# Kernel optimization log

Hardware: AMD Instinct MI355X
Metric: run time of the kernel (lower is better)

The kernel has to match this reference:

```python
import jax, jax.numpy as jnp
import numpy as np

B, S, D = 2, 2048, 4096
H, KV = 32, 8
HD = D // H  # 128
REP = H // KV  # 4
THETA = 10000.0


def _rope(x, cos, sin):
    # x: [B, S, N, HD]; cos/sin: [S, HD//2]
    xs = x.reshape(*x.shape[:-1], HD // 2, 2)
    x0, x1 = xs[..., 0], xs[..., 1]
    c = cos[None, :, None, :]
    s = sin[None, :, None, :]
    r0 = x0 * c - x1 * s
    r1 = x0 * s + x1 * c
    return jnp.stack([r0, r1], axis=-1).reshape(x.shape)


def setup_inputs() -> dict:
    key = jax.random.key(0)
    kx, kq, kk, kv, ko = jax.random.split(key, 5)
    x = jax.random.normal(kx, (B, S, D), dtype=jnp.float32)
    # faithful rope frequencies (precompute_freqs_cis equivalent)
    inv_freq = 1.0 / (THETA ** (np.arange(0, HD, 2, dtype=np.float32) / HD))
    freqs = np.outer(np.arange(S, dtype=np.float32), inv_freq)  # [S, HD//2]
    freqs_cos = jnp.asarray(np.cos(freqs))
    freqs_sin = jnp.asarray(np.sin(freqs))
    std = 0.02
    wq = jax.random.normal(kq, (H * HD, D), dtype=jnp.float32) * std
    wk = jax.random.normal(kk, (KV * HD, D), dtype=jnp.float32) * std
    wv = jax.random.normal(kv, (KV * HD, D), dtype=jnp.float32) * std
    wo = jax.random.normal(ko, (D, H * HD), dtype=jnp.float32) * std
    return {"x": x, "freqs_cos": freqs_cos, "freqs_sin": freqs_sin,
            "wq": wq, "wk": wk, "wv": wv, "wo": wo}


def reference(x, freqs_cos, freqs_sin, wq, wk, wv, wo):
    bs, seqlen, _ = x.shape
    q = (x @ wq.T).reshape(bs, seqlen, H, HD)
    k = (x @ wk.T).reshape(bs, seqlen, KV, HD)
    v = (x @ wv.T).reshape(bs, seqlen, KV, HD)
    q = _rope(q, freqs_cos, freqs_sin)
    k = _rope(k, freqs_cos, freqs_sin)
    # GQA: group query heads by kv head instead of materializing repeat_kv
    qg = q.reshape(bs, seqlen, KV, REP, HD)
    scale = 1.0 / jnp.sqrt(jnp.float32(HD))
    scores = jnp.einsum("bqgrd,bkgd->bgrqk", qg, k) * scale  # [B,KV,REP,S,S]
    causal = jnp.tril(jnp.ones((seqlen, seqlen), dtype=bool))
    scores = jnp.where(causal, scores, -jnp.inf)
    probs = jax.nn.softmax(scores, axis=-1)
    out = jnp.einsum("bgrqk,bkgd->bqgrd", probs, v)  # [B,S,KV,REP,HD]
    out = out.reshape(bs, seqlen, H * HD)
    return out @ wo.T
```

## Files before the change

### kernel.cpp

```cpp
#include <hip/hip_runtime.h>
#include <hip/hip_bf16.h>

#define BB 2
#define SS 2048
#define DD 4096
#define HH 32
#define KVH 8
#define HDD 128

using bf16 = __hip_bfloat16;
typedef __attribute__((ext_vector_type(8))) __bf16 bf16x8;
typedef __attribute__((ext_vector_type(4))) float f32x4;

#define GLOAD16(gp, lp) __builtin_amdgcn_global_load_lds(                     \
    (const __attribute__((address_space(1))) void*)(gp),                      \
    (__attribute__((address_space(3))) void*)(lp), 16, 0, 0)

__global__ __launch_bounds__(256) void cast_kernel(
    const float* __restrict__ s, bf16* __restrict__ d, int n4) {
  int i = blockIdx.x * blockDim.x + threadIdx.x;
  if (i >= n4) return;
  float4 v = ((const float4*)s)[i];
  bf16 a0 = __float2bfloat16(v.x), a1 = __float2bfloat16(v.y);
  bf16 a2 = __float2bfloat16(v.z), a3 = __float2bfloat16(v.w);
  ushort4 u;
  u.x = reinterpret_cast<unsigned short&>(a0);
  u.y = reinterpret_cast<unsigned short&>(a1);
  u.z = reinterpret_cast<unsigned short&>(a2);
  u.w = reinterpret_cast<unsigned short&>(a3);
  ((ushort4*)d)[i] = u;
}

__global__ __launch_bounds__(256) void rope_kernel(
    bf16* __restrict__ qb, bf16* __restrict__ kb,
    const float* __restrict__ fc, const float* __restrict__ fs) {
  int idx = blockIdx.x * blockDim.x + threadIdx.x;
  const int QP = BB * SS * HH * (HDD / 2);
  const int KP = BB * SS * KVH * (HDD / 2);
  bf16* p;
  int s, i;
  if (idx < QP) {
    int hr = idx >> 6;
    s = (hr >> 5) & (SS - 1);
    i = idx & 63;
    p = qb + ((size_t)hr << 7) + (i << 1);
  } else {
    int j = idx - QP;
    if (j >= KP) return;
    int hr = j >> 6;
    s = (hr >> 3) & (SS - 1);
    i = j & 63;
    p = kb + ((size_t)hr << 7) + (i << 1);
  }
  float c = fc[s * 64 + i], sn = fs[s * 64 + i];
  float x0 = __bfloat162float(p[0]), x1 = __bfloat162float(p[1]);
  p[0] = __float2bfloat16(x0 * c - x1 * sn);
  p[1] = __float2bfloat16(x0 * sn + x1 * c);
}

template <int MODE>
__global__ __launch_bounds__(256, 2) void gemm_bt(
    const bf16* __restrict__ A, const bf16* __restrict__ Bm,
    void* __restrict__ C, int M, int N, int K) {
  __shared__ __attribute__((aligned(16))) bf16 As[128 * 64];
  __shared__ __attribute__((aligned(16))) bf16 Bs[128 * 64];
  const int m0 = blockIdx.y * 128, n0 = blockIdx.x * 128;
  const int t = threadIdx.x;
  const int lane = t & 63, w = t >> 6;
  const int wm = (w >> 1) * 64, wn = (w & 1) * 64;
  const int lr = lane & 15, quad = lane >> 4;

  const int srow = t >> 3;
  const int scol8 = ((t & 7) ^ (srow & 7)) * 8;
  const bf16* aSrc = A + (size_t)(m0 + srow) * K + scol8;
  const bf16* bSrc = Bm + (size_t)(n0 + srow) * K + scol8;
  bf16* aDst = As + t * 8;
  bf16* bDst = Bs + t * 8;

  const int sl[2] = {((0 * 4 + quad) ^ (lr & 7)) * 8, ((1 * 4 + quad) ^ (lr & 7)) * 8};

  f32x4 acc[4][4];
#pragma unroll
  for (int i = 0; i < 4; i++)
#pragma unroll
    for (int j = 0; j < 4; j++) acc[i][j] = (f32x4)0.0f;

  for (int k0 = 0; k0 < K; k0 += 64) {
#pragma unroll
    for (int i = 0; i < 4; i++) {
      GLOAD16(aSrc + i * 32 * K, aDst + i * 2048);
      GLOAD16(bSrc + i * 32 * K, bDst + i * 2048);
    }
    __syncthreads();
#pragma unroll
    for (int kk = 0; kk < 2; kk++) {
      bf16x8 af[4], bfv[4];
#pragma unroll
      for (int i = 0; i < 4; i++)
        af[i] = *(const bf16x8*)(As + (wm + i * 16 + lr) * 64 + sl[kk]);
#pragma unroll
      for (int j = 0; j < 4; j++)
        bfv[j] = *(const bf16x8*)(Bs + (wn + j * 16 + lr) * 64 + sl[kk]);
#pragma unroll
      for (int i = 0; i < 4; i++)
#pragma unroll
        for (int j = 0; j < 4; j++)
          acc[i][j] = __builtin_amdgcn_mfma_f32_16x16x32_bf16(af[i], bfv[j], acc[i][j], 0, 0, 0);
    }
    __syncthreads();
    aSrc += 64;
    bSrc += 64;
  }

#pragma unroll
  for (int i = 0; i < 4; i++)
#pragma unroll
    for (int j = 0; j < 4; j++)
#pragma unroll
      for (int r = 0; r < 4; r++) {
        int row = m0 + wm + i * 16 + quad * 4 + r;
        int col = n0 + wn + j * 16 + lr;
        float v = acc[i][j][r];
        if (MODE == 0) {
          ((bf16*)C)[(size_t)row * N + col] = __float2bfloat16(v);
        } else if (MODE == 1) {
          ((float*)C)[(size_t)row * N + col] = v;
        } else {
          int bb = row >> 11, s = row & (SS - 1);
          int kv = col >> 7, d = col & (HDD - 1);
          ((bf16*)C)[((size_t)(bb * KVH + kv) * HDD + d) * SS + s] = __float2bfloat16(v);
        }
      }
}

__global__ __launch_bounds__(256, 2) void flash_kernel(
    const bf16* __restrict__ q, const bf16* __restrict__ k,
    const bf16* __restrict__ vt, bf16* __restrict__ out) {
  __shared__ __attribute__((aligned(16))) bf16 Ks[64 * 128];
  __shared__ __attribute__((aligned(16))) bf16 Vs[128 * 64];
  __shared__ __attribute__((aligned(16))) bf16 Ps[64 * 72];
  const int qt = blockIdx.x, h = blockIdx.y, b = blockIdx.z;
  const int kv = h >> 2;
  const int t = threadIdx.x;
  const int lane = t & 63, w = t >> 6;
  const int lr = lane & 15, quad = lane >> 4;
  const int q0 = qt * 64;

  bf16x8 qf[4];
  {
    const bf16* qp = q + ((size_t)(b * SS + q0 + w * 16 + lr) * HH + h) * HDD + quad * 8;
#pragma unroll
    for (int c = 0; c < 4; c++) qf[c] = *(const bf16x8*)(qp + c * 32);
  }

  f32x4 oa[8];
#pragma unroll
  for (int i = 0; i < 8; i++) oa[i] = (f32x4)0.0f;
  float m_i[4] = {-1e30f, -1e30f, -1e30f, -1e30f};
  float l_i[4] = {0.f, 0.f, 0.f, 0.f};
  const float scale = 0.08838834764831845f;

  const int krow = t >> 4;
  const int kcol8 = ((t & 15) ^ (krow & 15)) * 8;
  const bf16* kSrc0 = k + ((size_t)(b * SS + krow) * KVH + kv) * HDD + kcol8;
  const int vrow = t >> 3;
  const int vcol8 = ((t & 7) ^ (vrow & 7)) * 8;
  const bf16* vSrc0 = vt + ((size_t)(b * KVH + kv) * HDD + vrow) * SS + vcol8;
  bf16* kDst = Ks + t * 8;
  bf16* vDst = Vs + t * 8;

  const int slV[2] = {((0 * 4 + quad) ^ (lr & 7)) * 8, ((1 * 4 + quad) ^ (lr & 7)) * 8};

  for (int kt = 0; kt <= qt; kt++) {
    const int kt0 = kt * 64;
    const bf16* kSrc = kSrc0 + (size_t)kt0 * (KVH * HDD);
    const bf16* vSrc = vSrc0 + kt0;
#pragma unroll
    for (int i = 0; i < 4; i++) {
      GLOAD16(kSrc + i * 16 * KVH * HDD, kDst + i * 2048);
      GLOAD16(vSrc + i * 32 * SS, vDst + i * 2048);
    }
    __syncthreads();

    f32x4 sc4[4];
#pragma unroll
    for (int ni = 0; ni < 4; ni++) sc4[ni] = (f32x4)0.0f;
#pragma unroll
    for (int c = 0; c < 4; c++) {
#pragma unroll
      for (int ni = 0; ni < 4; ni++) {
        int row = ni * 16 + lr;
        bf16x8 kf = *(const bf16x8*)(Ks + row * 128 + (((c * 4 + quad) ^ lr) * 8));
        sc4[ni] = __builtin_amdgcn_mfma_f32_16x16x32_bf16(qf[c], kf, sc4[ni], 0, 0, 0);
      }
    }

    float mx[4] = {-1e30f, -1e30f, -1e30f, -1e30f};
#pragma unroll
    for (int ni = 0; ni < 4; ni++)
#pragma unroll
      for (int r = 0; r < 4; r++) {
        float v = sc4[ni][r] * scale;
        int kidx = kt0 + ni * 16 + lr;
        int qidx = q0 + w * 16 + quad * 4 + r;
        v = (kidx > qidx) ? -1e30f : v;
        sc4[ni][r] = v;
        mx[r] = fmaxf(mx[r], v);
      }
#pragma unroll
    for (int off = 1; off < 16; off <<= 1)
#pragma unroll
      for (int r = 0; r < 4; r++) mx[r] = fmaxf(mx[r], __shfl_xor(mx[r], off));

    float alpha[4], rs[4];
#pragma unroll
    for (int r = 0; r < 4; r++) {
      float mn = fmaxf(m_i[r], mx[r]);
      alpha[r] = __expf(m_i[r] - mn);
      m_i[r] = mn;
      rs[r] = 0.f;
    }
#pragma unroll
    for (int ni = 0; ni < 4; ni++)
#pragma unroll
      for (int r = 0; r < 4; r++) {
        float p = __expf(sc4[ni][r] - m_i[r]);
        sc4[ni][r] = p;
        rs[r] += p;
      }
#pragma unroll
    for (int off = 1; off < 16; off <<= 1)
#pragma unroll
      for (int r = 0; r < 4; r++) rs[r] += __shfl_xor(rs[r], off);
#pragma unroll
    for (int r = 0; r < 4; r++) l_i[r] = l_i[r] * alpha[r] + rs[r];
#pragma unroll
    for (int ni = 0; ni < 8; ni++)
#pragma unroll
      for (int r = 0; r < 4; r++) oa[ni][r] *= alpha[r];

#pragma unroll
    for (int ni = 0; ni < 4; ni++)
#pragma unroll
      for (int r = 0; r < 4; r++)
        Ps[(w * 16 + quad * 4 + r) * 72 + ni * 16 + lr] = __float2bfloat16(sc4[ni][r]);

#pragma unroll
    for (int kk = 0; kk < 2; kk++) {
      bf16x8 pf = *(const bf16x8*)(Ps + (w * 16 + lr) * 72 + kk * 32 + quad * 8);
#pragma unroll
      for (int ni = 0; ni < 8; ni++) {
        bf16x8 vf = *(const bf16x8*)(Vs + (ni * 16 + lr) * 64 + slV[kk]);
        oa[ni] = __builtin_amdgcn_mfma_f32_16x16x32_bf16(pf, vf, oa[ni], 0, 0, 0);
      }
    }
    __syncthreads();
  }

#pragma unroll
  for (int r = 0; r < 4; r++) {
    float inv = 1.0f / l_i[r];
    int srow = q0 + w * 16 + quad * 4 + r;
#pragma unroll
    for (int ni = 0; ni < 8; ni++) {
      int col = ni * 16 + lr;
      out[(size_t)(b * SS + srow) * DD + h * HDD + col] =
          __float2bfloat16(oa[ni][r] * inv);
    }
  }
}

extern "C" void kernel_launch(void* const* d_in, const int* in_sizes, int n_in,
                              void* d_out, int out_size, void* d_ws, size_t ws_size,
                              hipStream_t stream) {
  (void)in_sizes; (void)n_in; (void)out_size; (void)ws_size;
  const float* x  = (const float*)d_in[0];
  const float* fc = (const float*)d_in[1];
  const float* fs = (const float*)d_in[2];
  const float* wq = (const float*)d_in[3];
  const float* wk = (const float*)d_in[4];
  const float* wv = (const float*)d_in[5];
  const float* wo = (const float*)d_in[6];

  char* ws = (char*)d_ws;
  bf16* xb   = (bf16*)(ws);
  bf16* W    = (bf16*)(ws + (size_t)33554432);
  bf16* qb   = (bf16*)(ws + (size_t)67108864);
  bf16* kb   = (bf16*)(ws + (size_t)100663296);
  bf16* vtb  = (bf16*)(ws + (size_t)109051904);
  bf16* attn = xb;

  const int NX  = BB * SS * DD;
  const int NW  = DD * DD;
  const int NWK = KVH * HDD * DD;

  cast_kernel<<<NX / 1024, 256, 0, stream>>>(x, xb, NX / 4);
  cast_kernel<<<NW / 1024, 256, 0, stream>>>(wq, W, NW / 4);
  gemm_bt<0><<<dim3(32, 32), 256, 0, stream>>>(xb, W, qb, BB * SS, DD, DD);
  cast_kernel<<<NWK / 1024, 256, 0, stream>>>(wk, W, NWK / 4);
  gemm_bt<0><<<dim3(8, 32), 256, 0, stream>>>(xb, W, kb, BB * SS, KVH * HDD, DD);
  cast_kernel<<<NWK / 1024, 256, 0, stream>>>(wv, W, NWK / 4);
  gemm_bt<2><<<dim3(8, 32), 256, 0, stream>>>(xb, W, vtb, BB * SS, KVH * HDD, DD);
  rope_kernel<<<(BB * SS * (HH + KVH) * 64) / 256, 256, 0, stream>>>(qb, kb, fc, fs);
  flash_kernel<<<dim3(SS / 64, HH, BB), 256, 0, stream>>>(qb, kb, vtb, attn);
  cast_kernel<<<NW / 1024, 256, 0, stream>>>(wo, W, NW / 4);
  gemm_bt<1><<<dim3(32, 32), 256, 0, stream>>>(attn, W, (float*)d_out, BB * SS, DD, DD);
}
```

Measured before the change: 958.8 us.

## Enlarge flash attention query tile to 128 rows with reversed block order

The flash attention kernel now processes 128 query rows per block, with each wave handling two 16-row fragments. Each K/V tile loaded into shared memory is reused across twice as many queries, and K fragments are loaded once per chunk for both fragments. Blocks run in reverse order so the longest causal tiles start first. The softmax scale is folded into Q up front, and the causal mask is applied only on diagonal tiles. The cost is higher register pressure (doubled accumulators), a larger Ps buffer, half as many blocks, and some extra rounding from pre-scaling Q in bf16.

New measurement: 858.5 us. 10.5% less time.

```diff
diff --git a/kernel.cpp b/kernel.cpp
--- a/kernel.cpp
+++ b/kernel.cpp
@@ -138,27 +138,41 @@
     const bf16* __restrict__ vt, bf16* __restrict__ out) {
   __shared__ __attribute__((aligned(16))) bf16 Ks[64 * 128];
   __shared__ __attribute__((aligned(16))) bf16 Vs[128 * 64];
-  __shared__ __attribute__((aligned(16))) bf16 Ps[64 * 72];
-  const int qt = blockIdx.x, h = blockIdx.y, b = blockIdx.z;
+  __shared__ __attribute__((aligned(16))) bf16 Ps[128 * 72];
+  const int qt = gridDim.x - 1 - blockIdx.x;
+  const int h = blockIdx.y, b = blockIdx.z;
   const int kv = h >> 2;
   const int t = threadIdx.x;
   const int lane = t & 63, w = t >> 6;
   const int lr = lane & 15, quad = lane >> 4;
-  const int q0 = qt * 64;
-
-  bf16x8 qf[4];
-  {
-    const bf16* qp = q + ((size_t)(b * SS + q0 + w * 16 + lr) * HH + h) * HDD + quad * 8;
-#pragma unroll
-    for (int c = 0; c < 4; c++) qf[c] = *(const bf16x8*)(qp + c * 32);
+  const int q0 = qt * 128;
+  const int wr = w * 32;
+
+  bf16x8 qf[2][4];
+#pragma unroll
+  for (int mf = 0; mf < 2; mf++) {
+    const bf16* qp =
+        q + ((size_t)(b * SS + q0 + wr + mf * 16 + lr) * HH + h) * HDD + quad * 8;
+#pragma unroll
+    for (int c = 0; c < 4; c++) qf[mf][c] = *(const bf16x8*)(qp + c * 32);
   }
-
-  f32x4 oa[8];
-#pragma unroll
-  for (int i = 0; i < 8; i++) oa[i] = (f32x4)0.0f;
-  float m_i[4] = {-1e30f, -1e30f, -1e30f, -1e30f};
-  float l_i[4] = {0.f, 0.f, 0.f, 0.f};
   const float scale = 0.08838834764831845f;
+#pragma unroll
+  for (int mf = 0; mf < 2; mf++)
+#pragma unroll
+    for (int c = 0; c < 4; c++)
+#pragma unroll
+      for (int j = 0; j < 8; j++)
+        qf[mf][c][j] = (__bf16)((float)qf[mf][c][j] * scale);
+
+  f32x4 oa[2][8];
+#pragma unroll
+  for (int mf = 0; mf < 2; mf++)
+#pragma unroll
+    for (int i = 0; i < 8; i++) oa[mf][i] = (f32x4)0.0f;
+  float m_i[8], l_i[8];
+#pragma unroll
+  for (int r = 0; r < 8; r++) { m_i[r] = -1e30f; l_i[r] = 0.f; }
 
   const int krow = t >> 4;
   const int kcol8 = ((t & 15) ^ (krow & 15)) * 8;
@@ -171,7 +185,8 @@
 
   const int slV[2] = {((0 * 4 + quad) ^ (lr & 7)) * 8, ((1 * 4 + quad) ^ (lr & 7)) * 8};
 
-  for (int kt = 0; kt <= qt; kt++) {
+  const int nkt = 2 * qt + 2;
+  for (int kt = 0; kt < nkt; kt++) {
     const int kt0 = kt * 64;
     const bf16* kSrc = kSrc0 + (size_t)kt0 * (KVH * HDD);
     const bf16* vSrc = vSrc0 + kt0;
@@ -182,92 +197,122 @@
     }
     __syncthreads();
 
-    f32x4 sc4[4];
-#pragma unroll
-    for (int ni = 0; ni < 4; ni++) sc4[ni] = (f32x4)0.0f;
+    f32x4 sc[2][4];
+#pragma unroll
+    for (int mf = 0; mf < 2; mf++)
+#pragma unroll
+      for (int ni = 0; ni < 4; ni++) sc[mf][ni] = (f32x4)0.0f;
 #pragma unroll
     for (int c = 0; c < 4; c++) {
-#pragma unroll
-      for (int ni = 0; ni < 4; ni++) {
-        int row = ni * 16 + lr;
-        bf16x8 kf = *(const bf16x8*)(Ks + row * 128 + (((c * 4 + quad) ^ lr) * 8));
-        sc4[ni] = __builtin_amdgcn_mfma_f32_16x16x32_bf16(qf[c], kf, sc4[ni], 0, 0, 0);
-      }
-    }
-
-    float mx[4] = {-1e30f, -1e30f, -1e30f, -1e30f};
-#pragma unroll
-    for (int ni = 0; ni < 4; ni++)
-#pragma unroll
-      for (int r = 0; r < 4; r++) {
-        float v = sc4[ni][r] * scale;
-        int kidx = kt0 + ni * 16 + lr;
-        int qidx = q0 + w * 16 + quad * 4 + r;
-        v = (kidx > qidx) ? -1e30f : v;
-        sc4[ni][r] = v;
-        mx[r] = fmaxf(mx[r], v);
-      }
+      bf16x8 kf[4];
+#pragma unroll
+      for (int ni = 0; ni < 4; ni++)
+        kf[ni] = *(const bf16x8*)(Ks + (ni * 16 + lr) * 128 + (((c * 4 + quad) ^ lr) * 8));
+#pragma unroll
+      for (int mf = 0; mf < 2; mf++)
+#pragma unroll
+        for (int ni = 0; ni < 4; ni++)
+          sc[mf][ni] = __builtin_amdgcn_mfma_f32_16x16x32_bf16(qf[mf][c], kf[ni], sc[mf][ni], 0, 0, 0);
+    }
+
+    if (kt0 + 63 > q0 + wr) {
+#pragma unroll
+      for (int mf = 0; mf < 2; mf++)
+#pragma unroll
+        for (int ni = 0; ni < 4; ni++)
+#pragma unroll
+          for (int r = 0; r < 4; r++) {
+            int kidx = kt0 + ni * 16 + lr;
+            int qidx = q0 + wr + mf * 16 + quad * 4 + r;
+            if (kidx > qidx) sc[mf][ni][r] = -1e30f;
+          }
+    }
+
+    float mx[8];
+#pragma unroll
+    for (int r = 0; r < 8; r++) mx[r] = -1e30f;
+#pragma unroll
+    for (int mf = 0; mf < 2; mf++)
+#pragma unroll
+      for (int ni = 0; ni < 4; ni++)
+#pragma unroll
+        for (int r = 0; r < 4; r++)
+          mx[mf * 4 + r] = fmaxf(mx[mf * 4 + r], sc[mf][ni][r]);
 #pragma unroll
     for (int off = 1; off < 16; off <<= 1)
 #pragma unroll
-      for (int r = 0; r < 4; r++) mx[r] = fmaxf(mx[r], __shfl_xor(mx[r], off));
-
-    float alpha[4], rs[4];
-#pragma unroll
-    for (int r = 0; r < 4; r++) {
+      for (int r = 0; r < 8; r++) mx[r] = fmaxf(mx[r], __shfl_xor(mx[r], off));
+
+    float alpha[8], rs[8];
+#pragma unroll
+    for (int r = 0; r < 8; r++) {
       float mn = fmaxf(m_i[r], mx[r]);
       alpha[r] = __expf(m_i[r] - mn);
       m_i[r] = mn;
       rs[r] = 0.f;
     }
 #pragma unroll
-    for (int ni = 0; ni < 4; ni++)
-#pragma unroll
-      for (int r = 0; r < 4; r++) {
-        float p = __expf(sc4[ni][r] - m_i[r]);
-        sc4[ni][r] = p;
-        rs[r] += p;
-      }
+    for (int mf = 0; mf < 2; mf++)
+#pragma unroll
+      for (int ni = 0; ni < 4; ni++)
+#pragma unroll
+        for (int r = 0; r < 4; r++) {
+          float p = __expf(sc[mf][ni][r] - m_i[mf * 4 + r]);
+          sc[mf][ni][r] = p;
+          rs[mf * 4 + r] += p;
+        }
 #pragma unroll
     for (int off = 1; off < 16; off <<= 1)
 #pragma unroll
-      for (int r = 0; r < 4; r++) rs[r] += __shfl_xor(rs[r], off);
-#pragma unroll
-    for (int r = 0; r < 4; r++) l_i[r] = l_i[r] * alpha[r] + rs[r];
-#pragma unroll
-    for (int ni = 0; ni < 8; ni++)
-#pragma unroll
-      for (int r = 0; r < 4; r++) oa[ni][r] *= alpha[r];
-
-#pragma unroll
-    for (int ni = 0; ni < 4; ni++)
-#pragma unroll
-      for (int r = 0; r < 4; r++)
-        Ps[(w * 16 + quad * 4 + r) * 72 + ni * 16 + lr] = __float2bfloat16(sc4[ni][r]);
+      for (int r = 0; r < 8; r++) rs[r] += __shfl_xor(rs[r], off);
+#pragma unroll
+    for (int r = 0; r < 8; r++) l_i[r] = l_i[r] * alpha[r] + rs[r];
+#pragma unroll
+    for (int mf = 0; mf < 2; mf++)
+#pragma unroll
+      for (int ni = 0; ni < 8; ni++)
+#pragma unroll
+        for (int r = 0; r < 4; r++) oa[mf][ni][r] *= alpha[mf * 4 + r];
+
+#pragma unroll
+    for (int mf = 0; mf < 2; mf++)
+#pragma unroll
+      for (int ni = 0; ni < 4; ni++)
+#pragma unroll
+        for (int r = 0; r < 4; r++)
+          Ps[(wr + mf * 16 + quad * 4 + r) * 72 + ni * 16 + lr] =
+              __float2bfloat16(sc[mf][ni][r]);
 
 #pragma unroll
     for (int kk = 0; kk < 2; kk++) {
-      bf16x8 pf = *(const bf16x8*)(Ps + (w * 16 + lr) * 72 + kk * 32 + quad * 8);
+      bf16x8 pf[2];
+#pragma unroll
+      for (int mf = 0; mf < 2; mf++)
+        pf[mf] = *(const bf16x8*)(Ps + (wr + mf * 16 + lr) * 72 + kk * 32 + quad * 8);
 #pragma unroll
       for (int ni = 0; ni < 8; ni++) {
         bf16x8 vf = *(const bf16x8*)(Vs + (ni * 16 + lr) * 64 + slV[kk]);
-        oa[ni] = __builtin_amdgcn_mfma_f32_16x16x32_bf16(pf, vf, oa[ni], 0, 0, 0);
+#pragma unroll
+        for (int mf = 0; mf < 2; mf++)
+          oa[mf][ni] = __builtin_amdgcn_mfma_f32_16x16x32_bf16(pf[mf], vf, oa[mf][ni], 0, 0, 0);
       }
     }
     __syncthreads();
   }
 
 #pragma unroll
-  for (int r = 0; r < 4; r++) {
-    float inv = 1.0f / l_i[r];
-    int srow = q0 + w * 16 + quad * 4 + r;
-#pragma unroll
-    for (int ni = 0; ni < 8; ni++) {
-      int col = ni * 16 + lr;
-      out[(size_t)(b * SS + srow) * DD + h * HDD + col] =
-          __float2bfloat16(oa[ni][r] * inv);
-    }
-  }
+  for (int mf = 0; mf < 2; mf++)
+#pragma unroll
+    for (int r = 0; r < 4; r++) {
+      float inv = 1.0f / l_i[mf * 4 + r];
+      int srow = q0 + wr + mf * 16 + quad * 4 + r;
+#pragma unroll
+      for (int ni = 0; ni < 8; ni++) {
+        int col = ni * 16 + lr;
+        out[(size_t)(b * SS + srow) * DD + h * HDD + col] =
+            __float2bfloat16(oa[mf][ni][r] * inv);
+      }
+    }
 }
 
 extern "C" void kernel_launch(void* const* d_in, const int* in_sizes, int n_in,
@@ -302,7 +347,7 @@
   cast_kernel<<<NWK / 1024, 256, 0, stream>>>(wv, W, NWK / 4);
   gemm_bt<2><<<dim3(8, 32), 256, 0, stream>>>(xb, W, vtb, BB * SS, KVH * HDD, DD);
   rope_kernel<<<(BB * SS * (HH + KVH) * 64) / 256, 256, 0, stream>>>(qb, kb, fc, fs);
-  flash_kernel<<<dim3(SS / 64, HH, BB), 256, 0, stream>>>(qb, kb, vtb, attn);
+  flash_kernel<<<dim3(SS / 128, HH, BB), 256, 0, stream>>>(qb, kb, vtb, attn);
   cast_kernel<<<NW / 1024, 256, 0, stream>>>(wo, W, NW / 4);
   gemm_bt<1><<<dim3(32, 32), 256, 0, stream>>>(attn, W, (float*)d_out, BB * SS, DD, DD);
 }
```
